# Kernel optimization log

Measured on AMD Instinct MI355X. Metric: run time of the kernel, lower is better.

The kernel has to match this reference:

```python
import jax, jax.numpy as jnp
import numpy as np

HIDDEN = 256
HEADS = 8
HEAD_DIM = HIDDEN // HEADS
NUM_RBF = 32
CUTOFF = 8.0
K_PTS = 4096   # total points (32 molecules x 128)
N_ATOMS = 2048 # total atoms  (32 molecules x 64)
B_MOL = 32


def setup_inputs() -> dict:
    key = jax.random.key(0)
    ks = jax.random.split(key, 12)
    s = 0.02
    return {
        "h_point": jax.random.normal(ks[0], (K_PTS, HIDDEN), jnp.float32),
        "h_atom": jax.random.normal(ks[1], (N_ATOMS, HIDDEN), jnp.float32),
        "pos_point": jax.random.uniform(ks[2], (K_PTS, 3), jnp.float32) * 10.0,
        "pos_atom": jax.random.uniform(ks[3], (N_ATOMS, 3), jnp.float32) * 10.0,
        "Wq": jax.random.normal(ks[4], (HIDDEN, HIDDEN), jnp.float32) * s,
        "bq": jnp.zeros((HIDDEN,), jnp.float32),
        "Wk": jax.random.normal(ks[5], (HIDDEN, HIDDEN), jnp.float32) * s,
        "bk": jnp.zeros((HIDDEN,), jnp.float32),
        "Wv": jax.random.normal(ks[6], (HIDDEN, HIDDEN), jnp.float32) * s,
        "bv": jnp.zeros((HIDDEN,), jnp.float32),
        "Wo": jax.random.normal(ks[7], (HIDDEN, HIDDEN), jnp.float32) * s,
        "bo": jnp.zeros((HIDDEN,), jnp.float32),
        "W_rbf": jax.random.normal(ks[8], (NUM_RBF, HEADS), jnp.float32) * 0.1,
        "b_rbf": jnp.zeros((HEADS,), jnp.float32),
        "centers": jnp.linspace(0.0, CUTOFF, NUM_RBF, dtype=jnp.float32),
        "gamma": jnp.ones((HIDDEN,), jnp.float32),
        "beta": jnp.zeros((HIDDEN,), jnp.float32),
        "point_batch": jnp.repeat(jnp.arange(B_MOL), K_PTS // B_MOL),
        "atom_batch": jnp.repeat(jnp.arange(B_MOL), N_ATOMS // B_MOL),
    }


def reference(h_point, h_atom, pos_point, pos_atom,
              Wq, bq, Wk, bk, Wv, bv, Wo, bo,
              W_rbf, b_rbf, centers, gamma, beta,
              point_batch, atom_batch):
    H, D = HEADS, HEAD_DIM
    Kp = h_point.shape[0]
    Na = h_atom.shape[0]
    scale = D ** -0.5
    width = (CUTOFF / NUM_RBF) ** 2

    q = (h_point @ Wq + bq).reshape(Kp, H, D)
    k = (h_atom @ Wk + bk).reshape(Na, H, D)
    v = (h_atom @ Wv + bv).reshape(Na, H, D)

    # pairwise distances [Kp, Na]
    d2 = jnp.sum((pos_point[:, None, :] - pos_atom[None, :, :]) ** 2, axis=-1)
    dist = jnp.sqrt(jnp.maximum(d2, 0.0))

    # RBF distance bias -> [H, Kp, Na]
    rbf = jnp.exp(-((dist[..., None] - centers) ** 2) / width)  # [Kp, Na, NUM_RBF]
    bias = (rbf @ W_rbf + b_rbf).transpose(2, 0, 1)

    scores = jnp.einsum('khd,nhd->hkn', q, k) * scale + bias
    # ragged structure: point j only attends to atoms in the same molecule
    mask = point_batch[:, None] == atom_batch[None, :]  # [Kp, Na]
    scores = jnp.where(mask[None], scores, -1e30)
    attn = jax.nn.softmax(scores, axis=-1)

    agg = jnp.einsum('hkn,nhd->khd', attn, v).reshape(Kp, H * D)
    agg = agg @ Wo + bo

    x = h_point + agg
    mean = jnp.mean(x, axis=-1, keepdims=True)
    var = jnp.mean((x - mean) ** 2, axis=-1, keepdims=True)
    return (x - mean) * jax.lax.rsqrt(var + 1e-5) * gamma + beta
```

## Files before the change

### kernel.cpp

```cpp
#include <hip/hip_runtime.h>
#include <hip/hip_bf16.h>

#define HIDDEN 256
#define HEADS 8
#define HEAD_DIM 32
#define NUM_RBF 32
#define K_PTS 4096
#define N_ATOMS 2048
#define B_MOL 32
#define ATOMS_PER_MOL (N_ATOMS / B_MOL)

typedef __attribute__((ext_vector_type(8))) short bf16x8;
typedef __attribute__((ext_vector_type(4))) float f32x4;

__global__ __launch_bounds__(256) void prepW_kernel(
    const float* __restrict__ Wq, const float* __restrict__ Wk,
    const float* __restrict__ Wv, const float* __restrict__ Wo,
    __hip_bfloat16* __restrict__ WqT, __hip_bfloat16* __restrict__ WkT,
    __hip_bfloat16* __restrict__ WvT, __hip_bfloat16* __restrict__ WoT) {
    __shared__ float tile[32][33];
    const int t = blockIdx.x, tid = threadIdx.x;
    const int matId = t >> 6, tileId = t & 63;
    const int tr = (tileId >> 3) * 32, tc = (tileId & 7) * 32;
    const float* __restrict__ Ws = (matId == 0) ? Wq : (matId == 1) ? Wk : (matId == 2) ? Wv : Wo;
    __hip_bfloat16* __restrict__ Wd = (matId == 0) ? WqT : (matId == 1) ? WkT : (matId == 2) ? WvT : WoT;

    const int r = tid >> 3, cq = (tid & 7) * 4;
    const float4 in = *(const float4*)&Ws[(size_t)(tr + r) * HIDDEN + tc + cq];
    tile[r][cq + 0] = in.x; tile[r][cq + 1] = in.y;
    tile[r][cq + 2] = in.z; tile[r][cq + 3] = in.w;
    __syncthreads();
    __hip_bfloat16 o[4];
    o[0] = __float2bfloat16(tile[cq + 0][r]);
    o[1] = __float2bfloat16(tile[cq + 1][r]);
    o[2] = __float2bfloat16(tile[cq + 2][r]);
    o[3] = __float2bfloat16(tile[cq + 3][r]);
    *(uint2*)(Wd + (size_t)(tc + r) * HIDDEN + tr + cq) = *(const uint2*)o;
}

__device__ __forceinline__ bf16x8 cvt8(const float* p) {
    const float4 lo = *(const float4*)p;
    const float4 hi = *(const float4*)(p + 4);
    __hip_bfloat16 t[8];
    t[0] = __float2bfloat16(lo.x); t[1] = __float2bfloat16(lo.y);
    t[2] = __float2bfloat16(lo.z); t[3] = __float2bfloat16(lo.w);
    t[4] = __float2bfloat16(hi.x); t[5] = __float2bfloat16(hi.y);
    t[6] = __float2bfloat16(hi.z); t[7] = __float2bfloat16(hi.w);
    return *(const bf16x8*)t;
}

__global__ __launch_bounds__(256) void qkv3_kernel(
    const float* __restrict__ hp, const float* __restrict__ ha,
    const __hip_bfloat16* __restrict__ WqT, const float* __restrict__ bq, __hip_bfloat16* __restrict__ qb,
    const __hip_bfloat16* __restrict__ WkT, const float* __restrict__ bk, __hip_bfloat16* __restrict__ kb,
    const __hip_bfloat16* __restrict__ WvT, const float* __restrict__ bv, __hip_bfloat16* __restrict__ vtm) {
    const bool isQ = (blockIdx.x < 256);
    const float* __restrict__ A = isQ ? hp : ha;
    const __hip_bfloat16* __restrict__ W0T = isQ ? WqT : WkT;
    const float* __restrict__ b0 = isQ ? bq : bk;
    const int r0 = (isQ ? blockIdx.x : blockIdx.x - 256) * 16;

    const int wave = threadIdx.x >> 6, lane = threadIdx.x & 63;
    const int c0 = wave * 64;
    const int lrow = lane & 15, kgrp = lane >> 4;

    bf16x8 af[8];
    const float* Arow = A + (size_t)(r0 + lrow) * HIDDEN + kgrp * 8;
#pragma unroll
    for (int ks = 0; ks < 8; ++ks)
        af[ks] = cvt8(Arow + ks * 32);

    f32x4 acc0[4], acc1[4];
#pragma unroll
    for (int cc = 0; cc < 4; ++cc) {
        acc0[cc] = (f32x4){0.f, 0.f, 0.f, 0.f};
        acc1[cc] = (f32x4){0.f, 0.f, 0.f, 0.f};
    }

#pragma unroll
    for (int cc = 0; cc < 4; ++cc) {
        const short* W0r = (const short*)W0T + (size_t)(c0 + cc * 16 + lrow) * HIDDEN + kgrp * 8;
#pragma unroll
        for (int ks = 0; ks < 8; ++ks)
            acc0[cc] = __builtin_amdgcn_mfma_f32_16x16x32_bf16(
                af[ks], *(const bf16x8*)(W0r + ks * 32), acc0[cc], 0, 0, 0);
        if (!isQ) {
            const short* W1r = (const short*)WvT + (size_t)(c0 + cc * 16 + lrow) * HIDDEN + kgrp * 8;
#pragma unroll
            for (int ks = 0; ks < 8; ++ks)
                acc1[cc] = __builtin_amdgcn_mfma_f32_16x16x32_bf16(
                    af[ks], *(const bf16x8*)(W1r + ks * 32), acc1[cc], 0, 0, 0);
        }
    }

    const int colb = lane & 15;
    const int rowb = (lane >> 4) * 4;
#pragma unroll
    for (int cc = 0; cc < 4; ++cc) {
        const int cgl = c0 + cc * 16 + colb;
        const float bias0 = b0[cgl];
        if (isQ) {
#pragma unroll
            for (int rg = 0; rg < 4; ++rg)
                qb[(size_t)(r0 + rowb + rg) * HIDDEN + cgl] = __float2bfloat16(acc0[cc][rg] + bias0);
        } else {
            const float bias1 = bv[cgl];
            const int mol = r0 >> 6;
            const int abase = (r0 & 63) + rowb;
            __hip_bfloat16 vo[4];
#pragma unroll
            for (int rg = 0; rg < 4; ++rg) {
                kb[(size_t)(r0 + rowb + rg) * HIDDEN + cgl] = __float2bfloat16(acc0[cc][rg] + bias0);
                vo[rg] = __float2bfloat16(acc1[cc][rg] + bias1);
            }
            *(uint2*)(vtm + (size_t)mol * (HIDDEN * ATOMS_PER_MOL) +
                      (size_t)cgl * ATOMS_PER_MOL + abase) = *(const uint2*)vo;
        }
    }
}

#define AGG_PAD (HIDDEN + 16)

__global__ __launch_bounds__(512, 8) void attn_mfma8_kernel(
    const __hip_bfloat16* __restrict__ qb, const __hip_bfloat16* __restrict__ kb,
    const __hip_bfloat16* __restrict__ vtm,
    const float* __restrict__ pos_point, const float* __restrict__ pos_atom,
    const float* __restrict__ W_rbf, const float* __restrict__ b_rbf,
    const float* __restrict__ centers,
    const int* __restrict__ point_batch, const int* __restrict__ atom_batch,
    const __hip_bfloat16* __restrict__ WoT, const float* __restrict__ bo,
    const float* __restrict__ h_point,
    const float* __restrict__ gamma, const float* __restrict__ beta,
    float* __restrict__ out) {
    __shared__ float wrbf_lds[NUM_RBF][HEADS];
    __shared__ float cent_lds[NUM_RBF];
    __shared__ float brbf_lds[HEADS];
    __shared__ float bias_lds[HEADS][ATOMS_PER_MOL + 1][8];
    __shared__ __hip_bfloat16 p_lds[HEADS][8][72];
    __shared__ __hip_bfloat16 agg_lds[8][AGG_PAD];
    __shared__ float x_lds[8][260];
    __shared__ float red_s[8][4];
    __shared__ float red_q[8][4];

    const int tid = threadIdx.x, wave = tid >> 6, lane = tid & 63;
    const int j0 = blockIdx.x * 8;
    const float scale = 0.17677669529663687f;

    if (tid < NUM_RBF * HEADS) ((float*)wrbf_lds)[tid] = W_rbf[tid];
    if (tid < NUM_RBF) cent_lds[tid] = centers[tid];
    if (tid < HEADS) brbf_lds[tid] = b_rbf[tid];
    if (tid < 64) bias_lds[tid >> 3][ATOMS_PER_MOL][tid & 7] = 0.0f;
    __syncthreads();

    const int m = point_batch[j0];
    const int mbase = m * ATOMS_PER_MOL;

    {
        const int n = mbase + lane;
        const bool valid = (atom_batch[n] == m);
        const int j = j0 + wave;

        const float dx = pos_point[j * 3 + 0] - pos_atom[n * 3 + 0];
        const float dy = pos_point[j * 3 + 1] - pos_atom[n * 3 + 1];
        const float dz = pos_point[j * 3 + 2] - pos_atom[n * 3 + 2];
        const float dist = sqrtf(fmaxf(dx * dx + dy * dy + dz * dz, 0.0f));

        float bias[HEADS];
#pragma unroll
        for (int h = 0; h < HEADS; ++h) bias[h] = brbf_lds[h];
#pragma unroll
        for (int r = 0; r < NUM_RBF; ++r) {
            const float dd = dist - cent_lds[r];
            const float e = __expf(-16.0f * dd * dd);
#pragma unroll
            for (int h = 0; h < HEADS; ++h)
                bias[h] += e * wrbf_lds[r][h];
        }
#pragma unroll
        for (int h = 0; h < HEADS; ++h)
            bias_lds[h][lane][wave] = valid ? bias[h] : -1e30f;
    }
    __syncthreads();

    const int c = lane & 15, kgrp = lane >> 4;
    const int h = wave;
    {
        const bf16x8 aq = *(const bf16x8*)((const short*)qb +
                          (size_t)(j0 + (c & 7)) * HIDDEN + h * HEAD_DIM + kgrp * 8);

        f32x4 sacc[4];
#pragma unroll
        for (int t = 0; t < 4; ++t) {
            const bf16x8 bk_ = *(const bf16x8*)((const short*)kb +
                               (size_t)(mbase + c + 16 * t) * HIDDEN + h * HEAD_DIM + kgrp * 8);
            sacc[t] = __builtin_amdgcn_mfma_f32_16x16x32_bf16(
                aq, bk_, (f32x4){0.f, 0.f, 0.f, 0.f}, 0, 0, 0);
        }

        float s[4][4];
#pragma unroll
        for (int t = 0; t < 4; ++t) {
            const f32x4 bv = *(const f32x4*)&bias_lds[h][c + 16 * t][kgrp * 4];
#pragma unroll
            for (int r = 0; r < 4; ++r)
                s[t][r] = sacc[t][r] * scale + bv[r];
        }
#pragma unroll
        for (int r = 0; r < 4; ++r) {
            float mx = fmaxf(fmaxf(s[0][r], s[1][r]), fmaxf(s[2][r], s[3][r]));
#pragma unroll
            for (int off = 1; off <= 8; off <<= 1)
                mx = fmaxf(mx, __shfl_xor(mx, off));
            float e0 = __expf(s[0][r] - mx);
            float e1 = __expf(s[1][r] - mx);
            float e2 = __expf(s[2][r] - mx);
            float e3 = __expf(s[3][r] - mx);
            float ss = e0 + e1 + e2 + e3;
#pragma unroll
            for (int off = 1; off <= 8; off <<= 1)
                ss += __shfl_xor(ss, off);
            const float inv = 1.0f / ss;
            if (kgrp < 2) {
                const int pt = kgrp * 4 + r;
                p_lds[h][pt][c + 16 * 0] = __float2bfloat16(e0 * inv);
                p_lds[h][pt][c + 16 * 1] = __float2bfloat16(e1 * inv);
                p_lds[h][pt][c + 16 * 2] = __float2bfloat16(e2 * inv);
                p_lds[h][pt][c + 16 * 3] = __float2bfloat16(e3 * inv);
            }
        }

        const short* vbase = (const short*)vtm + (size_t)m * (HIDDEN * ATOMS_PER_MOL);
#pragma unroll
        for (int t2 = 0; t2 < 2; ++t2) {
            f32x4 pacc = (f32x4){0.f, 0.f, 0.f, 0.f};
#pragma unroll
            for (int ks = 0; ks < 2; ++ks) {
                const bf16x8 ap = *(const bf16x8*)&p_lds[h][c & 7][ks * 32 + kgrp * 8];
                const bf16x8 bvv = *(const bf16x8*)(vbase +
                                   (size_t)(h * HEAD_DIM + t2 * 16 + c) * ATOMS_PER_MOL +
                                   ks * 32 + kgrp * 8);
                pacc = __builtin_amdgcn_mfma_f32_16x16x32_bf16(ap, bvv, pacc, 0, 0, 0);
            }
            if (kgrp < 2) {
#pragma unroll
                for (int r = 0; r < 4; ++r)
                    agg_lds[kgrp * 4 + r][h * HEAD_DIM + t2 * 16 + c] = __float2bfloat16(pacc[r]);
            }
        }
    }
    __syncthreads();

    const int c0 = wave * 32;
    const int lrow = lane & 15, kgrp2 = lane >> 4;
    bf16x8 af[8];
    const bf16x8 zf = {0, 0, 0, 0, 0, 0, 0, 0};
#pragma unroll
    for (int ks = 0; ks < 8; ++ks)
        af[ks] = (lrow < 8) ? *(const bf16x8*)(&agg_lds[lrow & 7][kgrp2 * 8 + ks * 32]) : zf;

    f32x4 oacc[2];
#pragma unroll
    for (int cc = 0; cc < 2; ++cc) oacc[cc] = (f32x4){0.f, 0.f, 0.f, 0.f};
#pragma unroll
    for (int cc = 0; cc < 2; ++cc) {
        const short* Wr = (const short*)WoT + (size_t)(c0 + cc * 16 + lrow) * HIDDEN + kgrp2 * 8;
#pragma unroll
        for (int ks = 0; ks < 8; ++ks)
            oacc[cc] = __builtin_amdgcn_mfma_f32_16x16x32_bf16(
                af[ks], *(const bf16x8*)(Wr + ks * 32), oacc[cc], 0, 0, 0);
    }

    const int colb = lane & 15;
    const int rowb = (lane >> 4) * 4;
#pragma unroll
    for (int cc = 0; cc < 2; ++cc) {
        const int cgl = c0 + cc * 16 + colb;
        const float bias_o = bo[cgl];
#pragma unroll
        for (int rg = 0; rg < 4; ++rg) {
            const int rl = rowb + rg;
            if (rl < 8)
                x_lds[rl][cgl] = oacc[cc][rg] + bias_o + h_point[(size_t)(j0 + rl) * HIDDEN + cgl];
        }
    }
    __syncthreads();

    const int col = tid & 255;
    const int half = tid >> 8;
    const int ln = col & 63, wv = col >> 6;
    float xv[4];
#pragma unroll
    for (int r = 0; r < 4; ++r) {
        const int rr = half * 4 + r;
        xv[r] = x_lds[rr][col];
        float s = xv[r], qq = xv[r] * xv[r];
#pragma unroll
        for (int off = 32; off > 0; off >>= 1) {
            s += __shfl_xor(s, off);
            qq += __shfl_xor(qq, off);
        }
        if (ln == 0) { red_s[rr][wv] = s; red_q[rr][wv] = qq; }
    }
    __syncthreads();

    const float gc = gamma[col], bc = beta[col];
#pragma unroll
    for (int r = 0; r < 4; ++r) {
        const int rr = half * 4 + r;
        const float mean = (red_s[rr][0] + red_s[rr][1] + red_s[rr][2] + red_s[rr][3]) * (1.0f / HIDDEN);
        const float ex2  = (red_q[rr][0] + red_q[rr][1] + red_q[rr][2] + red_q[rr][3]) * (1.0f / HIDDEN);
        const float var = ex2 - mean * mean;
        out[(size_t)(j0 + rr) * HIDDEN + col] = (xv[r] - mean) * rsqrtf(var + 1e-5f) * gc + bc;
    }
}

extern "C" void kernel_launch(void* const* d_in, const int* in_sizes, int n_in,
                              void* d_out, int out_size, void* d_ws, size_t ws_size,
                              hipStream_t stream) {
    const float* h_point   = (const float*)d_in[0];
    const float* h_atom    = (const float*)d_in[1];
    const float* pos_point = (const float*)d_in[2];
    const float* pos_atom  = (const float*)d_in[3];
    const float* Wq        = (const float*)d_in[4];
    const float* bq        = (const float*)d_in[5];
    const float* Wk        = (const float*)d_in[6];
    const float* bk        = (const float*)d_in[7];
    const float* Wv        = (const float*)d_in[8];
    const float* bv        = (const float*)d_in[9];
    const float* Wo        = (const float*)d_in[10];
    const float* bo        = (const float*)d_in[11];
    const float* W_rbf     = (const float*)d_in[12];
    const float* b_rbf     = (const float*)d_in[13];
    const float* centers   = (const float*)d_in[14];
    const float* gamma     = (const float*)d_in[15];
    const float* beta      = (const float*)d_in[16];
    const int*   point_batch = (const int*)d_in[17];
    const int*   atom_batch  = (const int*)d_in[18];
    float* out = (float*)d_out;

    __hip_bfloat16* qb = (__hip_bfloat16*)d_ws;
    __hip_bfloat16* kb = qb + (size_t)K_PTS * HIDDEN;
    __hip_bfloat16* vtm = kb + (size_t)N_ATOMS * HIDDEN;
    __hip_bfloat16* WqT = vtm + (size_t)HIDDEN * N_ATOMS;
    __hip_bfloat16* WkT = WqT + HIDDEN * HIDDEN;
    __hip_bfloat16* WvT = WkT + HIDDEN * HIDDEN;
    __hip_bfloat16* WoT = WvT + HIDDEN * HIDDEN;

    prepW_kernel<<<256, 256, 0, stream>>>(Wq, Wk, Wv, Wo, WqT, WkT, WvT, WoT);

    qkv3_kernel<<<384, 256, 0, stream>>>(h_point, h_atom,
                                         WqT, bq, qb,
                                         WkT, bk, kb,
                                         WvT, bv, vtm);

    attn_mfma8_kernel<<<K_PTS / 8, 512, 0, stream>>>(qb, kb, vtm,
                                                     pos_point, pos_atom,
                                                     W_rbf, b_rbf, centers,
                                                     point_batch, atom_batch,
                                                     WoT, bo, h_point, gamma, beta,
                                                     out);
}
```

Baseline: 134.8 us.

## Move RBF distance-bias computation into QKV projection kernel as extra blocks

The RBF distance-bias evaluation moves out of the attention kernel into 512 extra blocks of the QKV projection launch. These blocks write the bias to a global workspace, and the attention kernel loads it into LDS with float4 copies. The aim is to run the bias work alongside the projection GEMMs and make the attention kernel shorter, leaving it fewer registers and LDS. In exchange it adds an 8 MB global write and read round-trip for the bias and grows the workspace.

Measured after the change: 138.1 us. +2.4%, slower.

```diff
diff --git a/kernel.cpp b/kernel.cpp
--- a/kernel.cpp
+++ b/kernel.cpp
@@ -49,18 +49,72 @@
     return *(const bf16x8*)t;
 }
 
-__global__ __launch_bounds__(256) void qkv3_kernel(
+__global__ __launch_bounds__(256) void qkv_bias_kernel(
     const float* __restrict__ hp, const float* __restrict__ ha,
     const __hip_bfloat16* __restrict__ WqT, const float* __restrict__ bq, __hip_bfloat16* __restrict__ qb,
     const __hip_bfloat16* __restrict__ WkT, const float* __restrict__ bk, __hip_bfloat16* __restrict__ kb,
-    const __hip_bfloat16* __restrict__ WvT, const float* __restrict__ bv, __hip_bfloat16* __restrict__ vtm) {
-    const bool isQ = (blockIdx.x < 256);
+    const __hip_bfloat16* __restrict__ WvT, const float* __restrict__ bv, __hip_bfloat16* __restrict__ vtm,
+    const float* __restrict__ pos_point, const float* __restrict__ pos_atom,
+    const float* __restrict__ W_rbf, const float* __restrict__ b_rbf,
+    const float* __restrict__ centers,
+    const int* __restrict__ point_batch, const int* __restrict__ atom_batch,
+    float* __restrict__ bias_g) {
+    const int b = blockIdx.x, tid = threadIdx.x;
+
+    if (b >= 384) {
+        __shared__ float wrbf_s[NUM_RBF][HEADS];
+        __shared__ float cent_s[NUM_RBF];
+        __shared__ float brbf_s[HEADS];
+        if (tid < NUM_RBF * HEADS) ((float*)wrbf_s)[tid] = W_rbf[tid];
+        if (tid < NUM_RBF) cent_s[tid] = centers[tid];
+        if (tid < HEADS) brbf_s[tid] = b_rbf[tid];
+        __syncthreads();
+
+        const int bb = b - 384;
+        const int j0 = bb * 8;
+        const int m = point_batch[j0];
+        const int mbase = m * ATOMS_PER_MOL;
+        float* bg = bias_g + (size_t)bb * (HEADS * ATOMS_PER_MOL * 8);
+
+#pragma unroll
+        for (int it = 0; it < 2; ++it) {
+            const int pair = tid + it * 256;
+            const int atom = pair >> 3;
+            const int pt = pair & 7;
+            const int n = mbase + atom;
+            const bool valid = (atom_batch[n] == m);
+            const int j = j0 + pt;
+
+            const float dx = pos_point[j * 3 + 0] - pos_atom[n * 3 + 0];
+            const float dy = pos_point[j * 3 + 1] - pos_atom[n * 3 + 1];
+            const float dz = pos_point[j * 3 + 2] - pos_atom[n * 3 + 2];
+            const float dist = sqrtf(fmaxf(dx * dx + dy * dy + dz * dz, 0.0f));
+
+            float bias[HEADS];
+#pragma unroll
+            for (int h = 0; h < HEADS; ++h) bias[h] = brbf_s[h];
+#pragma unroll
+            for (int r = 0; r < NUM_RBF; ++r) {
+                const float dd = dist - cent_s[r];
+                const float e = __expf(-16.0f * dd * dd);
+#pragma unroll
+                for (int h = 0; h < HEADS; ++h)
+                    bias[h] += e * wrbf_s[r][h];
+            }
+#pragma unroll
+            for (int h = 0; h < HEADS; ++h)
+                bg[h * (ATOMS_PER_MOL * 8) + atom * 8 + pt] = valid ? bias[h] : -1e30f;
+        }
+        return;
+    }
+
+    const bool isQ = (b < 256);
     const float* __restrict__ A = isQ ? hp : ha;
     const __hip_bfloat16* __restrict__ W0T = isQ ? WqT : WkT;
     const float* __restrict__ b0 = isQ ? bq : bk;
-    const int r0 = (isQ ? blockIdx.x : blockIdx.x - 256) * 16;
-
-    const int wave = threadIdx.x >> 6, lane = threadIdx.x & 63;
+    const int r0 = (isQ ? b : b - 256) * 16;
+
+    const int wave = tid >> 6, lane = tid & 63;
     const int c0 = wave * 64;
     const int lrow = lane & 15, kgrp = lane >> 4;
 
@@ -124,17 +178,12 @@
 __global__ __launch_bounds__(512, 8) void attn_mfma8_kernel(
     const __hip_bfloat16* __restrict__ qb, const __hip_bfloat16* __restrict__ kb,
     const __hip_bfloat16* __restrict__ vtm,
-    const float* __restrict__ pos_point, const float* __restrict__ pos_atom,
-    const float* __restrict__ W_rbf, const float* __restrict__ b_rbf,
-    const float* __restrict__ centers,
-    const int* __restrict__ point_batch, const int* __restrict__ atom_batch,
+    const float* __restrict__ bias_g,
+    const int* __restrict__ point_batch,
     const __hip_bfloat16* __restrict__ WoT, const float* __restrict__ bo,
     const float* __restrict__ h_point,
     const float* __restrict__ gamma, const float* __restrict__ beta,
     float* __restrict__ out) {
-    __shared__ float wrbf_lds[NUM_RBF][HEADS];
-    __shared__ float cent_lds[NUM_RBF];
-    __shared__ float brbf_lds[HEADS];
     __shared__ float bias_lds[HEADS][ATOMS_PER_MOL + 1][8];
     __shared__ __hip_bfloat16 p_lds[HEADS][8][72];
     __shared__ __hip_bfloat16 agg_lds[8][AGG_PAD];
@@ -146,41 +195,21 @@
     const int j0 = blockIdx.x * 8;
     const float scale = 0.17677669529663687f;
 
-    if (tid < NUM_RBF * HEADS) ((float*)wrbf_lds)[tid] = W_rbf[tid];
-    if (tid < NUM_RBF) cent_lds[tid] = centers[tid];
-    if (tid < HEADS) brbf_lds[tid] = b_rbf[tid];
-    if (tid < 64) bias_lds[tid >> 3][ATOMS_PER_MOL][tid & 7] = 0.0f;
+    {
+        const float* bg = bias_g + (size_t)blockIdx.x * (HEADS * ATOMS_PER_MOL * 8);
+#pragma unroll
+        for (int i = 0; i < 2; ++i) {
+            const int flat = (tid * 2 + i) * 4;
+            const int hh = flat >> 9;
+            const int rem = flat & 511;
+            *(float4*)((float*)bias_lds + hh * 520 + rem) = *(const float4*)(bg + flat);
+        }
+        if (tid < 64) bias_lds[tid >> 3][ATOMS_PER_MOL][tid & 7] = 0.0f;
+    }
     __syncthreads();
 
     const int m = point_batch[j0];
     const int mbase = m * ATOMS_PER_MOL;
-
-    {
-        const int n = mbase + lane;
-        const bool valid = (atom_batch[n] == m);
-        const int j = j0 + wave;
-
-        const float dx = pos_point[j * 3 + 0] - pos_atom[n * 3 + 0];
-        const float dy = pos_point[j * 3 + 1] - pos_atom[n * 3 + 1];
-        const float dz = pos_point[j * 3 + 2] - pos_atom[n * 3 + 2];
-        const float dist = sqrtf(fmaxf(dx * dx + dy * dy + dz * dz, 0.0f));
-
-        float bias[HEADS];
-#pragma unroll
-        for (int h = 0; h < HEADS; ++h) bias[h] = brbf_lds[h];
-#pragma unroll
-        for (int r = 0; r < NUM_RBF; ++r) {
-            const float dd = dist - cent_lds[r];
-            const float e = __expf(-16.0f * dd * dd);
-#pragma unroll
-            for (int h = 0; h < HEADS; ++h)
-                bias[h] += e * wrbf_lds[r][h];
-        }
-#pragma unroll
-        for (int h = 0; h < HEADS; ++h)
-            bias_lds[h][lane][wave] = valid ? bias[h] : -1e30f;
-    }
-    __syncthreads();
 
     const int c = lane & 15, kgrp = lane >> 4;
     const int h = wave;
@@ -345,18 +374,20 @@
     __hip_bfloat16* WkT = WqT + HIDDEN * HIDDEN;
     __hip_bfloat16* WvT = WkT + HIDDEN * HIDDEN;
     __hip_bfloat16* WoT = WvT + HIDDEN * HIDDEN;
+    float* bias_g = (float*)(WoT + HIDDEN * HIDDEN);
 
     prepW_kernel<<<256, 256, 0, stream>>>(Wq, Wk, Wv, Wo, WqT, WkT, WvT, WoT);
 
-    qkv3_kernel<<<384, 256, 0, stream>>>(h_point, h_atom,
-                                         WqT, bq, qb,
-                                         WkT, bk, kb,
-                                         WvT, bv, vtm);
+    qkv_bias_kernel<<<896, 256, 0, stream>>>(h_point, h_atom,
+                                             WqT, bq, qb,
+                                             WkT, bk, kb,
+                                             WvT, bv, vtm,
+                                             pos_point, pos_atom,
+                                             W_rbf, b_rbf, centers,
+                                             point_batch, atom_batch, bias_g);
 
     attn_mfma8_kernel<<<K_PTS / 8, 512, 0, stream>>>(qb, kb, vtm,
-                                                     pos_point, pos_atom,
-                                                     W_rbf, b_rbf, centers,
-                                                     point_batch, atom_batch,
+                                                     bias_g, point_batch,
                                                      WoT, bo, h_point, gamma, beta,
                                                      out);
 }
```
